# Kernel tuning notes

Measured on AMD Instinct MI355X. Metric: run time of the kernel, lower is better.

## Reference

```python
import jax, jax.numpy as jnp
import numpy as np

NUM_GAUSSIANS = 3  # coordinate dims per spot; nfeatures = 2*NG + 1 = 7


def setup_inputs() -> dict:
    key = jax.random.key(0)
    k1, k2 = jax.random.split(key)
    # uniform [0,1) keeps prob/sigma channels positive (module clamps anyway)
    features = jax.random.uniform(k1, (16, 16, 7, 64, 64), dtype=jnp.float32)
    targets = jax.random.uniform(k2, (16, 16, 32, 4), dtype=jnp.float32)
    return {"features": features, "targets": targets}


def reference(features, targets):
    ng = NUM_GAUSSIANS
    B, F, nf, h, w = features.shape
    max_spots = targets.shape[2]

    feat = features.reshape(-1, nf, h, w)             # (BF, 7, h, w)
    tgt = targets.reshape(-1, max_spots, ng + 1)      # (BF, S, ng+1)
    mask = tgt[..., 0]                                # (BF, S)
    true_values = tgt[..., 1:]                        # (BF, S, ng)

    prob = jnp.clip(feat[:, 0], 1e-20).reshape(-1, h * w)              # (BF, hw)
    mu = feat[:, 1:ng + 1].reshape(-1, ng, h * w)                      # (BF, ng, hw)
    sigma = jnp.clip(feat[:, 1 + ng:], 1e-10).reshape(-1, ng, h * w)   # (BF, ng, hw)

    logprob_norm = jnp.log(prob) - jnp.log(prob.sum(-1, keepdims=True))  # (BF, hw)

    # broadcast: (BF, S, ng, 1) vs (BF, 1, ng, hw) -> (BF, S, ng, hw)
    inputs = true_values[:, :, :, None]
    means = mu[:, None]
    sigmas = sigma[:, None]
    log_normal = -(inputs - means) ** 2 / (2.0 * sigmas ** 2) - jnp.log(sigmas)

    # sum over gaussian dims, logsumexp over spatial mixture components
    log_gmm_prob = jax.nn.logsumexp(logprob_norm[:, None] + log_normal.sum(2), axis=2)  # (BF, S)

    loss_gmm = jnp.sum(log_gmm_prob * mask, axis=-1)  # (BF,)
    return (-loss_gmm).reshape(B, F)
```

## Files before the change

### kernel.cpp

```cpp
#include <hip/hip_runtime.h>

#define NG 3
#define HW 4096
#define NB 256
#define NSPOT 32
#define NSPLIT 4
#define PXB (HW / NSPLIT)
#define TPB 256
#define PXT (PXB / TPB)
#define NPAIR (PXT / 2)
#define NWAVE (TPB / 64)

#define NHALF_LOG2E -0.7213475204444817f
#define LN2 0.6931471805599453f

typedef float f32x2 __attribute__((ext_vector_type(2)));

__global__ __launch_bounds__(TPB) void gmm_main(const float* __restrict__ feat,
                                                const float* __restrict__ tgt,
                                                float* __restrict__ wsS,
                                                float* __restrict__ wsP) {
    const int b = blockIdx.x >> 2;
    const int slice = blockIdx.x & 3;
    const int tid = threadIdx.x;
    const int lane = tid & 63;
    const int wv = tid >> 6;

    __shared__ float4 spot_tab[NSPOT];
    __shared__ float Ssh[NWAVE][NSPOT];
    __shared__ float Psh[NWAVE];

    if (tid < NSPOT) {
        const float* tb = tgt + (size_t)b * (NSPOT * 4) + tid * 4;
        spot_tab[tid] = make_float4(tb[1], tb[2], tb[3], 0.f);
    }
    __syncthreads();

    const float* fb = feat + (size_t)b * (7 * HW) + slice * PXB;
    const int p4 = tid * 4;

    float4 f0 = *(const float4*)(fb + 0 * HW + p4);
    float4 f1 = *(const float4*)(fb + 1 * HW + p4);
    float4 f2 = *(const float4*)(fb + 2 * HW + p4);
    float4 f3 = *(const float4*)(fb + 3 * HW + p4);
    float4 f4v = *(const float4*)(fb + 4 * HW + p4);
    float4 f5 = *(const float4*)(fb + 5 * HW + p4);
    float4 f6 = *(const float4*)(fb + 6 * HW + p4);

    float pr[PXT] = {f0.x, f0.y, f0.z, f0.w};
    float mu_s[NG][PXT] = {{f1.x, f1.y, f1.z, f1.w},
                           {f2.x, f2.y, f2.z, f2.w},
                           {f3.x, f3.y, f3.z, f3.w}};
    float sg_s[NG][PXT] = {{f4v.x, f4v.y, f4v.z, f4v.w},
                           {f5.x, f5.y, f5.z, f5.w},
                           {f6.x, f6.y, f6.z, f6.w}};

    float a_s[NG][PXT], c_s[PXT];
    float psum = 0.f;
#pragma unroll
    for (int k = 0; k < PXT; ++k) {
        float p = fmaxf(pr[k], 1e-20f);
        psum += p;
        float c2 = __builtin_amdgcn_logf(p);
#pragma unroll
        for (int g = 0; g < NG; ++g) {
            float s = fmaxf(sg_s[g][k], 1e-10f);
            c2 -= __builtin_amdgcn_logf(s);
            a_s[g][k] = NHALF_LOG2E * __builtin_amdgcn_rcpf(s * s);
        }
        c_s[k] = c2;
    }

    f32x2 MU[NG][NPAIR], A[NG][NPAIR], C[NPAIR];
#pragma unroll
    for (int pp = 0; pp < NPAIR; ++pp) {
        C[pp] = (f32x2){c_s[2 * pp], c_s[2 * pp + 1]};
#pragma unroll
        for (int g = 0; g < NG; ++g) {
            MU[g][pp] = (f32x2){mu_s[g][2 * pp], mu_s[g][2 * pp + 1]};
            A[g][pp] = (f32x2){a_s[g][2 * pp], a_s[g][2 * pp + 1]};
        }
    }

    float acc[NSPOT];
#pragma unroll
    for (int s = 0; s < NSPOT; ++s) {
        float4 t = spot_tab[s];
        f32x2 x[NPAIR];
#pragma unroll
        for (int pp = 0; pp < NPAIR; ++pp) {
            f32x2 x2 = C[pp];
            {
                f32x2 z = t.x - MU[0][pp];
                x2 += (z * A[0][pp]) * z;
            }
            {
                f32x2 z = t.y - MU[1][pp];
                x2 += (z * A[1][pp]) * z;
            }
            {
                f32x2 z = t.z - MU[2][pp];
                x2 += (z * A[2][pp]) * z;
            }
            x[pp] = x2;
        }
        float e0 = __builtin_amdgcn_exp2f(x[0].x) + __builtin_amdgcn_exp2f(x[0].y);
        float e1 = __builtin_amdgcn_exp2f(x[1].x) + __builtin_amdgcn_exp2f(x[1].y);
        acc[s] = e0 + e1;
    }

#define RSTEP(D, HALF)                                          \
    {                                                           \
        const bool hi = (lane & (D)) != 0;                      \
        _Pragma("unroll") for (int i = 0; i < (HALF); ++i) {    \
            float send = hi ? acc[i] : acc[i + (HALF)];         \
            float recv = __shfl_xor(send, (D), 64);             \
            acc[i] = (hi ? acc[i + (HALF)] : acc[i]) + recv;    \
        }                                                       \
    }
    RSTEP(32, 16)
    RSTEP(16, 8)
    RSTEP(8, 4)
    RSTEP(4, 2)
    RSTEP(2, 1)
#undef RSTEP
    acc[0] += __shfl_xor(acc[0], 1, 64);
    if ((lane & 1) == 0) Ssh[wv][lane >> 1] = acc[0];

    float ps = psum;
#pragma unroll
    for (int m = 1; m < 64; m <<= 1) ps += __shfl_xor(ps, m, 64);
    if (lane == 0) Psh[wv] = ps;
    __syncthreads();

    if (tid < NSPOT) {
        float tot = 0.f;
#pragma unroll
        for (int w = 0; w < NWAVE; ++w) tot += Ssh[w][tid];
        wsS[((size_t)b * NSPLIT + slice) * NSPOT + tid] = tot;
    }
    if (tid == NSPOT) {
        float tot = 0.f;
#pragma unroll
        for (int w = 0; w < NWAVE; ++w) tot += Psh[w];
        wsP[b * NSPLIT + slice] = tot;
    }
}

__global__ __launch_bounds__(64) void gmm_final(const float* __restrict__ tgt,
                                                const float* __restrict__ wsS,
                                                const float* __restrict__ wsP,
                                                float* __restrict__ out) {
    const int b = blockIdx.x;
    const int lane = threadIdx.x;

    float ps = (lane < NSPLIT) ? wsP[b * NSPLIT + lane] : 0.f;
#pragma unroll
    for (int m = 1; m < 64; m <<= 1) ps += __shfl_xor(ps, m, 64);

    float contrib = 0.f;
    if (lane < NSPOT) {
        float S = 0.f;
#pragma unroll
        for (int k = 0; k < NSPLIT; ++k)
            S += wsS[((size_t)b * NSPLIT + k) * NSPOT + lane];
        float mask = tgt[(size_t)b * (NSPOT * 4) + lane * 4];
        contrib = mask * (__builtin_amdgcn_logf(S) - __builtin_amdgcn_logf(ps));
    }
#pragma unroll
    for (int m = 1; m < 64; m <<= 1) contrib += __shfl_xor(contrib, m, 64);

    if (lane == 0) out[b] = -contrib * LN2;
}

extern "C" void kernel_launch(void* const* d_in, const int* in_sizes, int n_in,
                              void* d_out, int out_size, void* d_ws, size_t ws_size,
                              hipStream_t stream) {
    const float* feat = (const float*)d_in[0];
    const float* tgt = (const float*)d_in[1];
    float* out = (float*)d_out;

    float* wsS = (float*)d_ws;
    float* wsP = wsS + NB * NSPLIT * NSPOT;

    gmm_main<<<NB * NSPLIT, TPB, 0, stream>>>(feat, tgt, wsS, wsP);
    gmm_final<<<NB, 64, 0, stream>>>(tgt, wsS, wsP, out);
}
```

Measured before the change: 82.94 us.

## Fuse main and final kernels into one 1024-thread block per batch item

Each block now covers a whole frame's 4096 pixels with 1024 threads instead of splitting it across four 256-thread blocks. The final log and mask reduction therefore happens in-block, so the second kernel launch and the workspace round-trip are gone. The cost is fewer blocks (256 instead of 1024), which may reduce occupancy and latency hiding on the device. Large blocks with many live registers per thread could also limit how many waves each CU holds.

```diff
diff --git a/kernel.cpp b/kernel.cpp
--- a/kernel.cpp
+++ b/kernel.cpp
@@ -4,10 +4,8 @@
 #define HW 4096
 #define NB 256
 #define NSPOT 32
-#define NSPLIT 4
-#define PXB (HW / NSPLIT)
-#define TPB 256
-#define PXT (PXB / TPB)
+#define TPB 1024
+#define PXT 4
 #define NPAIR (PXT / 2)
 #define NWAVE (TPB / 64)
 
@@ -16,12 +14,10 @@
 
 typedef float f32x2 __attribute__((ext_vector_type(2)));
 
-__global__ __launch_bounds__(TPB) void gmm_main(const float* __restrict__ feat,
-                                                const float* __restrict__ tgt,
-                                                float* __restrict__ wsS,
-                                                float* __restrict__ wsP) {
-    const int b = blockIdx.x >> 2;
-    const int slice = blockIdx.x & 3;
+__global__ __launch_bounds__(TPB) void gmm_fused(const float* __restrict__ feat,
+                                                 const float* __restrict__ tgt,
+                                                 float* __restrict__ out) {
+    const int b = blockIdx.x;
     const int tid = threadIdx.x;
     const int lane = tid & 63;
     const int wv = tid >> 6;
@@ -36,7 +32,7 @@
     }
     __syncthreads();
 
-    const float* fb = feat + (size_t)b * (7 * HW) + slice * PXB;
+    const float* fb = feat + (size_t)b * (7 * HW);
     const int p4 = tid * 4;
 
     float4 f0 = *(const float4*)(fb + 0 * HW + p4);
@@ -133,44 +129,26 @@
     if (lane == 0) Psh[wv] = ps;
     __syncthreads();
 
-    if (tid < NSPOT) {
-        float tot = 0.f;
+    if (tid < 64) {
+        float contrib = 0.f, msum = 0.f;
+        if (tid < NSPOT) {
+            float S = 0.f;
 #pragma unroll
-        for (int w = 0; w < NWAVE; ++w) tot += Ssh[w][tid];
-        wsS[((size_t)b * NSPLIT + slice) * NSPOT + tid] = tot;
+            for (int w = 0; w < NWAVE; ++w) S += Ssh[w][tid];
+            float mask = tgt[(size_t)b * (NSPOT * 4) + tid * 4];
+            contrib = mask * __builtin_amdgcn_logf(S);
+            msum = mask;
+        }
+        float pv = (tid < NWAVE) ? Psh[tid] : 0.f;
+#pragma unroll
+        for (int m = 1; m < 64; m <<= 1) {
+            contrib += __shfl_xor(contrib, m, 64);
+            msum += __shfl_xor(msum, m, 64);
+            pv += __shfl_xor(pv, m, 64);
+        }
+        if (tid == 0)
+            out[b] = -LN2 * (contrib - msum * __builtin_amdgcn_logf(pv));
     }
-    if (tid == NSPOT) {
-        float tot = 0.f;
-#pragma unroll
-        for (int w = 0; w < NWAVE; ++w) tot += Psh[w];
-        wsP[b * NSPLIT + slice] = tot;
-    }
-}
-
-__global__ __launch_bounds__(64) void gmm_final(const float* __restrict__ tgt,
-                                                const float* __restrict__ wsS,
-                                                const float* __restrict__ wsP,
-                                                float* __restrict__ out) {
-    const int b = blockIdx.x;
-    const int lane = threadIdx.x;
-
-    float ps = (lane < NSPLIT) ? wsP[b * NSPLIT + lane] : 0.f;
-#pragma unroll
-    for (int m = 1; m < 64; m <<= 1) ps += __shfl_xor(ps, m, 64);
-
-    float contrib = 0.f;
-    if (lane < NSPOT) {
-        float S = 0.f;
-#pragma unroll
-        for (int k = 0; k < NSPLIT; ++k)
-            S += wsS[((size_t)b * NSPLIT + k) * NSPOT + lane];
-        float mask = tgt[(size_t)b * (NSPOT * 4) + lane * 4];
-        contrib = mask * (__builtin_amdgcn_logf(S) - __builtin_amdgcn_logf(ps));
-    }
-#pragma unroll
-    for (int m = 1; m < 64; m <<= 1) contrib += __shfl_xor(contrib, m, 64);
-
-    if (lane == 0) out[b] = -contrib * LN2;
 }
 
 extern "C" void kernel_launch(void* const* d_in, const int* in_sizes, int n_in,
@@ -180,9 +158,5 @@
     const float* tgt = (const float*)d_in[1];
     float* out = (float*)d_out;
 
-    float* wsS = (float*)d_ws;
-    float* wsP = wsS + NB * NSPLIT * NSPOT;
-
-    gmm_main<<<NB * NSPLIT, TPB, 0, stream>>>(feat, tgt, wsS, wsP);
-    gmm_final<<<NB, 64, 0, stream>>>(tgt, wsS, wsP, out);
+    gmm_fused<<<NB, TPB, 0, stream>>>(feat, tgt, out);
 }
```

Measured after the change: 80.52 us. 2.9% less time.
